# Performance work log

Measured on AMD Instinct MI355X. Metric: run time of the kernel, lower is better.

## Reference

```python
import jax, jax.numpy as jnp
import numpy as np

B, C, H, W = 2, 64, 64, 64
C2 = C // 2
N = H * W


def conv1x1(x, w, b):
    # x: (B,Cin,H,W), w: (Cout,Cin), b: (Cout,)
    return jnp.einsum('bchw,oc->bohw', x, w) + b[None, :, None, None]


def setup_inputs() -> dict:
    key = jax.random.key(0)
    ks = jax.random.split(key, 20)
    s = 0.05
    d = {
        'x1': jax.random.normal(ks[0], (B, C, H, W), jnp.float32),
        'x2': jax.random.normal(ks[1], (B, C, H, W), jnp.float32),
        'wq1': jax.random.normal(ks[2], (C2, C), jnp.float32) * s,
        'bq1': jax.random.normal(ks[3], (C2,), jnp.float32) * s,
        'wk1': jax.random.normal(ks[4], (C2, C), jnp.float32) * s,
        'bk1': jax.random.normal(ks[5], (C2,), jnp.float32) * s,
        'wv1': jax.random.normal(ks[6], (C2, C), jnp.float32) * s,
        'bv1': jax.random.normal(ks[7], (C2,), jnp.float32) * s,
        'wc1': jax.random.normal(ks[8], (C, C2), jnp.float32) * s,
        'bc1': jax.random.normal(ks[9], (C,), jnp.float32) * s,
        'wq2': jax.random.normal(ks[10], (C2, C), jnp.float32) * s,
        'bq2': jax.random.normal(ks[11], (C2,), jnp.float32) * s,
        'wk2': jax.random.normal(ks[12], (C2, C), jnp.float32) * s,
        'bk2': jax.random.normal(ks[13], (C2,), jnp.float32) * s,
        'wv2': jax.random.normal(ks[14], (C2, C), jnp.float32) * s,
        'bv2': jax.random.normal(ks[15], (C2,), jnp.float32) * s,
        'wc2': jax.random.normal(ks[16], (C, C2), jnp.float32) * s,
        'bc2': jax.random.normal(ks[17], (C,), jnp.float32) * s,
        'gamma1': jax.random.normal(ks[18], (1,), jnp.float32) * 0.5,
        'gamma2': jax.random.normal(ks[19], (1,), jnp.float32) * 0.5,
    }
    return d


def reference(x1, x2, wq1, bq1, wk1, bk1, wv1, bv1, wc1, bc1,
              wq2, bq2, wk2, bk2, wv2, bv2, wc2, bc2, gamma1, gamma2):
    b, c, h, w = x1.shape
    n = h * w
    # branch-1 projections (boundary semantics)
    q1 = jnp.max(conv1x1(x1, wq1, bq1), axis=1).reshape(b, n)          # (B,N) channel-max
    k1 = jnp.max(conv1x1(x1, wk1, bk1).reshape(b, -1, n), axis=1)      # (B,N)
    v1 = conv1x1(x1, wv1, bv1).reshape(b, -1, n)                        # (B,C/2,N)
    # branch-2 projections (field semantics)
    q2 = jnp.mean(conv1x1(x2, wq2, bq2), axis=1).reshape(b, n)         # (B,N) channel-mean
    k2 = jnp.mean(conv1x1(x2, wk2, bk2).reshape(b, -1, n), axis=1)     # (B,N)
    v2 = conv1x1(x2, wv2, bv2).reshape(b, -1, n)                        # (B,C/2,N)
    # energy2 = q1 (B,N,1) @ k2 (B,1,N) outer product; inverted sigmoid gate
    att2 = 1.0 - jax.nn.sigmoid(q1[:, :, None] * k2[:, None, :])        # (B,N,N)
    out1 = jnp.einsum('bck,bmk->bcm', v1, att2).reshape(b, c // 2, h, w)
    out1 = conv1x1(out1, wc2, bc2)
    # energy1 = q2 outer k1; sigmoid gate
    att1 = jax.nn.sigmoid(q2[:, :, None] * k1[:, None, :])              # (B,N,N)
    out2 = jnp.einsum('bck,bmk->bcm', v2, att1).reshape(b, c // 2, h, w)
    out2 = conv1x1(out2, wc1, bc1)
    out1 = x1 + gamma1[0] * out1
    out2 = x2 + gamma2[0] * out2
    return (out1, out2)
```

## Files before the change

### kernel.cpp

```cpp
#include <hip/hip_runtime.h>
#include <hip/hip_bf16.h>

#define NN 4096
#define CC 64
#define C2 32
#define BB 2

#define NSEG   4
#define M_BLK  64
#define KBLK   64
#define KB_ITERS (NN / NSEG / KBLK)

#define WS_Q1 0
#define WS_K1 8192
#define WS_Q2 16384
#define WS_K2 24576
#define WS_V1 32768
#define WS_V2 163840
#define WS_P  294912

typedef __attribute__((address_space(1))) const unsigned int GUI;
typedef __attribute__((address_space(3))) unsigned int LUI;
typedef __attribute__((ext_vector_type(8))) short bf16x8;
typedef __attribute__((ext_vector_type(4))) float f32x4;

__device__ __forceinline__ void glds16(const void* g, void* l) {
    __builtin_amdgcn_global_load_lds((GUI*)g, (LUI*)l, 16, 0, 0);
}

__device__ __forceinline__ unsigned short bf16_rne(float f) {
    union { float f; unsigned u; } x; x.f = f;
    unsigned u = x.u + 0x7fff + ((x.u >> 16) & 1);
    return (unsigned short)(u >> 16);
}
__device__ __forceinline__ unsigned pack2(float a, float b) {
    __hip_bfloat162 h = __float22bfloat162_rn(make_float2(a, b));
    unsigned r; __builtin_memcpy(&r, &h, 4); return r;
}
__device__ __forceinline__ float sigm_e2(float x) {
    return __builtin_amdgcn_rcpf(1.0f + __builtin_amdgcn_exp2f(x));
}

__global__ __launch_bounds__(256) void proj_kernel(
    const float* __restrict__ x1, const float* __restrict__ x2,
    const float* __restrict__ wq1, const float* __restrict__ bq1,
    const float* __restrict__ wk1, const float* __restrict__ bk1,
    const float* __restrict__ wv1, const float* __restrict__ bv1,
    const float* __restrict__ wq2, const float* __restrict__ bq2,
    const float* __restrict__ wk2, const float* __restrict__ bk2,
    const float* __restrict__ wv2, const float* __restrict__ bv2,
    float* __restrict__ ws)
{
    const int ln = threadIdx.x & 63;
    const int og = threadIdx.x >> 6;
    const int n  = blockIdx.x * 64 + ln;
    const int p  = blockIdx.y;
    const int b  = blockIdx.z;

    const float* x; const float* w; const float* bias;
    int mode; float* dstf; unsigned short* dstv;
    switch (p) {
      case 0: x = x1; w = wq1; bias = bq1; mode = 0; dstf = ws + WS_Q1; dstv = 0; break;
      case 1: x = x1; w = wk1; bias = bk1; mode = 0; dstf = ws + WS_K1; dstv = 0; break;
      case 2: x = x1; w = wv1; bias = bv1; mode = 2; dstf = 0; dstv = (unsigned short*)(ws + WS_V1); break;
      case 3: x = x2; w = wq2; bias = bq2; mode = 1; dstf = ws + WS_Q2; dstv = 0; break;
      case 4: x = x2; w = wk2; bias = bk2; mode = 1; dstf = ws + WS_K2; dstv = 0; break;
      default:x = x2; w = wv2; bias = bv2; mode = 2; dstf = 0; dstv = (unsigned short*)(ws + WS_V2); break;
    }

    __shared__ float red[4][C2][64];

    float acc[C2];
    #pragma unroll
    for (int o = 0; o < C2; ++o) acc[o] = 0.0f;

    const float* xb = x + ((size_t)b * CC + og * 16) * NN + n;
    #pragma unroll
    for (int ci = 0; ci < 16; ++ci) {
        const float xv = xb[(size_t)ci * NN];
        #pragma unroll
        for (int o = 0; o < C2; ++o)
            acc[o] += w[o * CC + og * 16 + ci] * xv;
    }
    #pragma unroll
    for (int o = 0; o < C2; ++o) red[og][o][ln] = acc[o];
    __syncthreads();

    float f[8];
    #pragma unroll
    for (int j = 0; j < 8; ++j) {
        const int o = og * 8 + j;
        f[j] = red[0][o][ln] + red[1][o][ln] + red[2][o][ln] + red[3][o][ln]
             + bias[o];
    }

    if (mode == 2) {
        #pragma unroll
        for (int j = 0; j < 8; ++j)
            dstv[((size_t)b * C2 + og * 8 + j) * NN + n] = bf16_rne(f[j]);
    } else {
        float r;
        if (mode == 0) {
            r = f[0];
            #pragma unroll
            for (int j = 1; j < 8; ++j) r = fmaxf(r, f[j]);
        } else {
            r = 0.0f;
            #pragma unroll
            for (int j = 0; j < 8; ++j) r += f[j];
        }
        __syncthreads();
        red[og][0][ln] = r;
        __syncthreads();
        if (og == 0) {
            const float a0 = red[0][0][ln], a1 = red[1][0][ln];
            const float a2 = red[2][0][ln], a3 = red[3][0][ln];
            const float rr = (mode == 0)
                ? fmaxf(fmaxf(a0, a1), fmaxf(a2, a3))
                : (a0 + a1 + a2 + a3) * (1.0f / C2);
            dstf[(size_t)b * NN + n] = rr;
        }
    }
}

__global__ __launch_bounds__(256) void attn_mfma(
    const float* __restrict__ q1, const float* __restrict__ k1,
    const float* __restrict__ q2, const float* __restrict__ k2,
    const unsigned short* __restrict__ v1, const unsigned short* __restrict__ v2,
    float* __restrict__ pout)
{
    __shared__ unsigned short vtile[2][C2 * KBLK];
    __shared__ unsigned short stile[2][M_BLK * KBLK];

    const int tid = threadIdx.x;
    const int wv  = tid >> 6;
    const int ln  = tid & 63;

    const int seg    = blockIdx.y;
    const int z      = blockIdx.z;
    const int branch = z & 1;
    const int b      = z >> 1;
    const int m0     = blockIdx.x * M_BLK;
    const int kstart = seg * (NN / NSEG);

    const float* q; const float* kv; const unsigned short* vbf; float sl2e;
    if (branch == 0) { q = q1; kv = k2; vbf = v1; sl2e =  1.44269504089f; }
    else             { q = q2; kv = k1; vbf = v2; sl2e = -1.44269504089f; }

    const float qs = q[(size_t)b * NN + m0 + ln] * sl2e;
    const float* kvb = kv + (size_t)b * NN;

    f32x4 acc[4];
    #pragma unroll
    for (int mt = 0; mt < 4; ++mt) acc[mt] = (f32x4){0.f, 0.f, 0.f, 0.f};

    const int vc = tid >> 3;
    const int vs = tid & 7;
    const unsigned short* vsrc0 = vbf + (size_t)(b * C2 + vc) * NN
                                + ((vs ^ (vc & 7)) << 3);

    auto sigPackWrite = [&](int buf, float4 ka, float4 kb4, float4 kc, float4 kd) {
        float s[16];
        s[0]  = sigm_e2(qs * ka.x);  s[1]  = sigm_e2(qs * ka.y);
        s[2]  = sigm_e2(qs * ka.z);  s[3]  = sigm_e2(qs * ka.w);
        s[4]  = sigm_e2(qs * kb4.x); s[5]  = sigm_e2(qs * kb4.y);
        s[6]  = sigm_e2(qs * kb4.z); s[7]  = sigm_e2(qs * kb4.w);
        s[8]  = sigm_e2(qs * kc.x);  s[9]  = sigm_e2(qs * kc.y);
        s[10] = sigm_e2(qs * kc.z);  s[11] = sigm_e2(qs * kc.w);
        s[12] = sigm_e2(qs * kd.x);  s[13] = sigm_e2(qs * kd.y);
        s[14] = sigm_e2(qs * kd.z);  s[15] = sigm_e2(qs * kd.w);

        uint4 w0, w1;
        w0.x = pack2(s[0],  s[1]);  w0.y = pack2(s[2],  s[3]);
        w0.z = pack2(s[4],  s[5]);  w0.w = pack2(s[6],  s[7]);
        w1.x = pack2(s[8],  s[9]);  w1.y = pack2(s[10], s[11]);
        w1.z = pack2(s[12], s[13]); w1.w = pack2(s[14], s[15]);

        char* srow = (char*)stile[buf] + ln * 128;
        *(uint4*)(srow + ((((wv << 1) | 0) ^ (ln & 7)) << 4)) = w0;
        *(uint4*)(srow + ((((wv << 1) | 1) ^ (ln & 7)) << 4)) = w1;
    };

    glds16(vsrc0 + kstart, (char*)vtile[0] + tid * 16);
    {
        const float* kvp = kvb + kstart + (wv << 4);
        sigPackWrite(0, *(const float4*)(kvp),     *(const float4*)(kvp + 4),
                        *(const float4*)(kvp + 8), *(const float4*)(kvp + 12));
    }
    asm volatile("s_waitcnt vmcnt(0)" ::: "memory");
    __syncthreads();

    const int ct  = wv & 1;
    const int ks  = wv >> 1;
    const int col = (ks << 2) + (ln >> 4);
    const int ac  = ct * 16 + (ln & 15);

    for (int kb = 0; kb < KB_ITERS; ++kb) {
        const int cur = kb & 1;
        const bool more = (kb + 1 < KB_ITERS);

        float4 ka, kb4, kc, kd;
        if (more) {
            glds16(vsrc0 + kstart + (kb + 1) * KBLK,
                   (char*)vtile[cur ^ 1] + tid * 16);
            const float* kvp = kvb + kstart + (kb + 1) * KBLK + (wv << 4);
            ka  = *(const float4*)(kvp);
            kb4 = *(const float4*)(kvp + 4);
            kc  = *(const float4*)(kvp + 8);
            kd  = *(const float4*)(kvp + 12);
        }

        const bf16x8 af = *(const bf16x8*)((const char*)vtile[cur]
                          + ac * 128 + ((col ^ (ac & 7)) << 4));
        #pragma unroll
        for (int mt = 0; mt < 4; ++mt) {
            const int bm = mt * 16 + (ln & 15);
            const bf16x8 bfr = *(const bf16x8*)((const char*)stile[cur]
                               + bm * 128 + ((col ^ (bm & 7)) << 4));
            acc[mt] = __builtin_amdgcn_mfma_f32_16x16x32_bf16(af, bfr, acc[mt], 0, 0, 0);
        }

        if (more) sigPackWrite(cur ^ 1, ka, kb4, kc, kd);

        asm volatile("s_waitcnt vmcnt(0)" ::: "memory");
        __syncthreads();
    }

    float* red = (float*)stile;
    if (wv >= 2) {
        #pragma unroll
        for (int mt = 0; mt < 4; ++mt)
            *(f32x4*)&red[((wv - 2) * 4 + mt) * 256 + ln * 4] = acc[mt];
    }
    __syncthreads();
    if (wv < 2) {
        const size_t obase = (((size_t)(branch * NSEG + seg) * BB + b) * C2) * NN;
        #pragma unroll
        for (int mt = 0; mt < 4; ++mt) {
            const f32x4 o = *(const f32x4*)&red[(wv * 4 + mt) * 256 + ln * 4];
            acc[mt].x += o.x; acc[mt].y += o.y; acc[mt].z += o.z; acc[mt].w += o.w;
            #pragma unroll
            for (int j = 0; j < 4; ++j) {
                const int c = wv * 16 + (ln >> 4) * 4 + j;
                const int m = m0 + mt * 16 + (ln & 15);
                pout[obase + (size_t)c * NN + m] = acc[mt][j];
            }
        }
    }
}

__global__ __launch_bounds__(256) void conv_kernel(
    const float* __restrict__ x1, const float* __restrict__ x2,
    const float* __restrict__ wc1, const float* __restrict__ bc1,
    const float* __restrict__ wc2, const float* __restrict__ bc2,
    const float* __restrict__ g1,  const float* __restrict__ g2,
    const float* __restrict__ p,   float* __restrict__ out)
{
    const int m      = blockIdx.x * 256 + threadIdx.x;
    const int co0    = blockIdx.y * 8;
    const int b      = blockIdx.z >> 1;
    const int branch = blockIdx.z & 1;

    const float* w; const float* bias; const float* x; float gamma; float* o;
    if (branch == 0) { w = wc2; bias = bc2; x = x1; gamma = g1[0]; o = out; }
    else             { w = wc1; bias = bc1; x = x2; gamma = g2[0]; o = out + (size_t)BB * CC * NN; }

    float s[C2];
    #pragma unroll
    for (int c = 0; c < C2; ++c) s[c] = 0.0f;

    #pragma unroll 1
    for (int seg = 0; seg < NSEG; ++seg) {
        const float* sb = p + (((size_t)(branch * NSEG + seg) * BB + b) * C2) * NN + m;
        #pragma unroll
        for (int c = 0; c < C2; ++c)
            s[c] += sb[(size_t)c * NN];
    }

    #pragma unroll
    for (int co = co0; co < co0 + 8; ++co) {
        float a = bias[co];
        #pragma unroll
        for (int c = 0; c < C2; ++c)
            a += w[co * C2 + c] * s[c];
        const size_t idx = ((size_t)b * CC + co) * NN + m;
        o[idx] = x[idx] + gamma * a;
    }
}

extern "C" void kernel_launch(void* const* d_in, const int* in_sizes, int n_in,
                              void* d_out, int out_size, void* d_ws, size_t ws_size,
                              hipStream_t stream)
{
    const float* x1  = (const float*)d_in[0];
    const float* x2  = (const float*)d_in[1];
    const float* wq1 = (const float*)d_in[2];
    const float* bq1 = (const float*)d_in[3];
    const float* wk1 = (const float*)d_in[4];
    const float* bk1 = (const float*)d_in[5];
    const float* wv1 = (const float*)d_in[6];
    const float* bv1 = (const float*)d_in[7];
    const float* wc1 = (const float*)d_in[8];
    const float* bc1 = (const float*)d_in[9];
    const float* wq2 = (const float*)d_in[10];
    const float* bq2 = (const float*)d_in[11];
    const float* wk2 = (const float*)d_in[12];
    const float* bk2 = (const float*)d_in[13];
    const float* wv2 = (const float*)d_in[14];
    const float* bv2 = (const float*)d_in[15];
    const float* wc2 = (const float*)d_in[16];
    const float* bc2 = (const float*)d_in[17];
    const float* g1  = (const float*)d_in[18];
    const float* g2  = (const float*)d_in[19];

    float* ws  = (float*)d_ws;
    float* out = (float*)d_out;

    proj_kernel<<<dim3(NN / 64, 6, BB), 256, 0, stream>>>(
        x1, x2, wq1, bq1, wk1, bk1, wv1, bv1,
        wq2, bq2, wk2, bk2, wv2, bv2, ws);

    const float* q1 = ws + WS_Q1; const float* k1 = ws + WS_K1;
    const float* q2 = ws + WS_Q2; const float* k2 = ws + WS_K2;
    const unsigned short* v1 = (const unsigned short*)(ws + WS_V1);
    const unsigned short* v2 = (const unsigned short*)(ws + WS_V2);
    float* pp = ws + WS_P;

    attn_mfma<<<dim3(NN / M_BLK, NSEG, BB * 2), 256, 0, stream>>>(
        q1, k1, q2, k2, v1, v2, pp);

    conv_kernel<<<dim3(NN / 256, 8, BB * 2), 256, 0, stream>>>(
        x1, x2, wc1, bc1, wc2, bc2, g1, g2, pp, out);
}
```

Measured before the change: 51.13 us.

## Retile attention MFMA kernel to 32-row M blocks with 128-wide K blocks

Changes the attention tile shape from 64x64 to M_BLK=32 and KBLK=128, which doubles the grid in the M dimension and halves the number of K iterations per block. The thread-to-sigmoid mapping, the V tile loads (two glds per thread) and the LDS swizzle are reworked for 256-byte rows, and each wave now issues two K-halves of MFMAs over two M tiles. The aim is more blocks for occupancy and fewer barrier round-trips per segment, in exchange for reloading the V tile across twice as many M blocks. Each block also does the same sigmoid work per element, now spread over 32 rows.

```diff
diff --git a/kernel.cpp b/kernel.cpp
--- a/kernel.cpp
+++ b/kernel.cpp
@@ -7,8 +7,8 @@
 #define BB 2
 
 #define NSEG   4
-#define M_BLK  64
-#define KBLK   64
+#define M_BLK  32
+#define KBLK   128
 #define KB_ITERS (NN / NSEG / KBLK)
 
 #define WS_Q1 0
@@ -39,6 +39,10 @@
 }
 __device__ __forceinline__ float sigm_e2(float x) {
     return __builtin_amdgcn_rcpf(1.0f + __builtin_amdgcn_exp2f(x));
+}
+
+__device__ __forceinline__ int swz(int slot, int row) {
+    return (slot & 8) | ((slot & 7) ^ (row & 7));
 }
 
 __global__ __launch_bounds__(256) void proj_kernel(
@@ -147,17 +151,20 @@
     if (branch == 0) { q = q1; kv = k2; vbf = v1; sl2e =  1.44269504089f; }
     else             { q = q2; kv = k1; vbf = v2; sl2e = -1.44269504089f; }
 
-    const float qs = q[(size_t)b * NN + m0 + ln] * sl2e;
+    const int sm = tid & 31;
+    const int sc = tid >> 5;
+    const float qs = q[(size_t)b * NN + m0 + sm] * sl2e;
     const float* kvb = kv + (size_t)b * NN;
 
-    f32x4 acc[4];
-    #pragma unroll
-    for (int mt = 0; mt < 4; ++mt) acc[mt] = (f32x4){0.f, 0.f, 0.f, 0.f};
-
-    const int vc = tid >> 3;
-    const int vs = tid & 7;
-    const unsigned short* vsrc0 = vbf + (size_t)(b * C2 + vc) * NN
-                                + ((vs ^ (vc & 7)) << 3);
+    f32x4 acc[2];
+    #pragma unroll
+    for (int mt = 0; mt < 2; ++mt) acc[mt] = (f32x4){0.f, 0.f, 0.f, 0.f};
+
+    const int vr = tid >> 4;
+    const int vs = tid & 15;
+    const unsigned short* vsrcA = vbf + ((size_t)b * C2 + vr) * NN
+                                + (size_t)swz(vs, vr) * 8;
+    const unsigned short* vsrcB = vsrcA + (size_t)16 * NN;
 
     auto sigPackWrite = [&](int buf, float4 ka, float4 kb4, float4 kc, float4 kd) {
         float s[16];
@@ -176,24 +183,24 @@
         w1.x = pack2(s[8],  s[9]);  w1.y = pack2(s[10], s[11]);
         w1.z = pack2(s[12], s[13]); w1.w = pack2(s[14], s[15]);
 
-        char* srow = (char*)stile[buf] + ln * 128;
-        *(uint4*)(srow + ((((wv << 1) | 0) ^ (ln & 7)) << 4)) = w0;
-        *(uint4*)(srow + ((((wv << 1) | 1) ^ (ln & 7)) << 4)) = w1;
+        char* srow = (char*)stile[buf] + sm * 256;
+        *(uint4*)(srow + (swz(sc * 2,     sm) << 4)) = w0;
+        *(uint4*)(srow + (swz(sc * 2 + 1, sm) << 4)) = w1;
     };
 
-    glds16(vsrc0 + kstart, (char*)vtile[0] + tid * 16);
+    glds16(vsrcA + kstart, (char*)vtile[0] + tid * 16);
+    glds16(vsrcB + kstart, (char*)vtile[0] + 4096 + tid * 16);
     {
-        const float* kvp = kvb + kstart + (wv << 4);
+        const float* kvp = kvb + kstart + sc * 16;
         sigPackWrite(0, *(const float4*)(kvp),     *(const float4*)(kvp + 4),
                         *(const float4*)(kvp + 8), *(const float4*)(kvp + 12));
     }
     asm volatile("s_waitcnt vmcnt(0)" ::: "memory");
     __syncthreads();
 
-    const int ct  = wv & 1;
-    const int ks  = wv >> 1;
-    const int col = (ks << 2) + (ln >> 4);
-    const int ac  = ct * 16 + (ln & 15);
+    const int ct = wv & 1;
+    const int ks = wv >> 1;
+    const int ac = ct * 16 + (ln & 15);
 
     for (int kb = 0; kb < KB_ITERS; ++kb) {
         const int cur = kb & 1;
@@ -201,23 +208,28 @@
 
         float4 ka, kb4, kc, kd;
         if (more) {
-            glds16(vsrc0 + kstart + (kb + 1) * KBLK,
-                   (char*)vtile[cur ^ 1] + tid * 16);
-            const float* kvp = kvb + kstart + (kb + 1) * KBLK + (wv << 4);
+            const int kn = kstart + (kb + 1) * KBLK;
+            glds16(vsrcA + kn, (char*)vtile[cur ^ 1] + tid * 16);
+            glds16(vsrcB + kn, (char*)vtile[cur ^ 1] + 4096 + tid * 16);
+            const float* kvp = kvb + kn + sc * 16;
             ka  = *(const float4*)(kvp);
             kb4 = *(const float4*)(kvp + 4);
             kc  = *(const float4*)(kvp + 8);
             kd  = *(const float4*)(kvp + 12);
         }
 
-        const bf16x8 af = *(const bf16x8*)((const char*)vtile[cur]
-                          + ac * 128 + ((col ^ (ac & 7)) << 4));
-        #pragma unroll
-        for (int mt = 0; mt < 4; ++mt) {
-            const int bm = mt * 16 + (ln & 15);
-            const bf16x8 bfr = *(const bf16x8*)((const char*)stile[cur]
-                               + bm * 128 + ((col ^ (bm & 7)) << 4));
-            acc[mt] = __builtin_amdgcn_mfma_f32_16x16x32_bf16(af, bfr, acc[mt], 0, 0, 0);
+        #pragma unroll
+        for (int kh = 0; kh < 2; ++kh) {
+            const int slot = ks * 8 + kh * 4 + (ln >> 4);
+            const bf16x8 af = *(const bf16x8*)((const char*)vtile[cur]
+                              + ac * 256 + (swz(slot, ac) << 4));
+            #pragma unroll
+            for (int mt = 0; mt < 2; ++mt) {
+                const int bm = mt * 16 + (ln & 15);
+                const bf16x8 bfr = *(const bf16x8*)((const char*)stile[cur]
+                                   + bm * 256 + (swz(slot, bm) << 4));
+                acc[mt] = __builtin_amdgcn_mfma_f32_16x16x32_bf16(af, bfr, acc[mt], 0, 0, 0);
+            }
         }
 
         if (more) sigPackWrite(cur ^ 1, ka, kb4, kc, kd);
@@ -229,15 +241,15 @@
     float* red = (float*)stile;
     if (wv >= 2) {
         #pragma unroll
-        for (int mt = 0; mt < 4; ++mt)
-            *(f32x4*)&red[((wv - 2) * 4 + mt) * 256 + ln * 4] = acc[mt];
+        for (int mt = 0; mt < 2; ++mt)
+            *(f32x4*)&red[((wv - 2) * 2 + mt) * 256 + ln * 4] = acc[mt];
     }
     __syncthreads();
     if (wv < 2) {
         const size_t obase = (((size_t)(branch * NSEG + seg) * BB + b) * C2) * NN;
         #pragma unroll
-        for (int mt = 0; mt < 4; ++mt) {
-            const f32x4 o = *(const f32x4*)&red[(wv * 4 + mt) * 256 + ln * 4];
+        for (int mt = 0; mt < 2; ++mt) {
+            const f32x4 o = *(const f32x4*)&red[(wv * 2 + mt) * 256 + ln * 4];
             acc[mt].x += o.x; acc[mt].y += o.y; acc[mt].z += o.z; acc[mt].w += o.w;
             #pragma unroll
             for (int j = 0; j < 4; ++j) {
@@ -329,6 +341,6 @@
     attn_mfma<<<dim3(NN / M_BLK, NSEG, BB * 2), 256, 0, stream>>>(
         q1, k1, q2, k2, v1, v2, pp);
 
-    conv_kernel<<<dim3(NN / 256, 8, BB * 2), 256, 0, stream>>>(
+    conv_kernel<<<dim3(NN / 256, CC / 8, BB * 2), 256, 0, stream>>>(
         x1, x2, wc1, bc1, wc2, bc2, g1, g2, pp, out);
 }
```

Result: slower. 52.50 us (+2.7%).
